# Optimization experiments

Measured on AMD Instinct MI355X. Metric: run time of the kernel, lower is better.

Reference implementation:

```python
import jax, jax.numpy as jnp
import numpy as np

B, S, D, E, K = 4, 2048, 1024, 8, 2


def setup_inputs() -> dict:
    key = jax.random.key(0)
    k1, k2, k3 = jax.random.split(key, 3)
    scale = 1.0 / np.sqrt(D)
    x = jax.random.normal(k1, (B, S, D), dtype=jnp.float32)
    Wg = jax.random.normal(k2, (D, E), dtype=jnp.float32) * scale
    bg = jnp.zeros((E,), dtype=jnp.float32)
    We = jax.random.normal(k3, (E, D, D), dtype=jnp.float32) * scale
    be = jnp.zeros((E, D), dtype=jnp.float32)
    return {"x": x, "Wg": Wg, "bg": bg, "We": We, "be": be}


def reference(x, Wg, bg, We, be):
    # gate scores: [B, S, E]
    gate_scores = jnp.einsum("bsd,de->bse", x, Wg) + bg
    topk_values, topk_indices = jax.lax.top_k(gate_scores, K)
    # mask: -inf everywhere except at top-k indices (where value == score)
    sel = jax.nn.one_hot(topk_indices, E, dtype=jnp.bool_).any(axis=-2)  # [B,S,E]
    masked = jnp.where(sel, gate_scores, -jnp.inf)
    gate_weights = jax.nn.softmax(masked, axis=-1)  # [B,S,E]
    # dense all-expert compute, as in the original: [B,S,E,D]
    expert_outputs = jnp.einsum("bsd,edh->bseh", x, We) + be
    fused = jnp.einsum("bse,bseh->bsh", gate_weights, expert_outputs)
    return fused
```

## Files before the change

kernel.cpp:

```cpp
#include <hip/hip_runtime.h>
#include <stdint.h>

#define NTOK   8192
#define DIM    1024
#define NEXP   8
#define MAXP   8192

#define BM 128
#define BN 128
#define BK 32

typedef float    f32x4  __attribute__((ext_vector_type(4)));
typedef __bf16   bf16x8 __attribute__((ext_vector_type(8)));
typedef _Float16 h16x8  __attribute__((ext_vector_type(8)));

typedef __attribute__((address_space(1))) const void* gas_ptr;
typedef __attribute__((address_space(3))) void*       las_ptr;

__device__ __forceinline__ unsigned short f32_to_bf16(float f) {
  union { float f; unsigned int u; } v; v.f = f;
  unsigned int u = v.u;
  unsigned int r = (u + 0x7FFFu + ((u >> 16) & 1u)) >> 16;
  return (unsigned short)r;
}

__global__ __launch_bounds__(256) void prep_kernel(
    const float* __restrict__ We, unsigned short* __restrict__ Wf,
    const float* __restrict__ x, const float* __restrict__ Wg,
    const float* __restrict__ bg, unsigned short* __restrict__ Xbf,
    int* __restrict__ tok_ee, float2* __restrict__ tok_w) {
  __shared__ float tile[64][65];
  const int bid = blockIdx.x;
  if (bid < 2048) {
    const int e  = bid >> 8;
    const int d0 = ((bid >> 4) & 15) * 64;
    const int h0 = (bid & 15) * 64;
    const int t  = threadIdx.x;
    const int tx = t & 63, ty = t >> 6;
    const float* src = We + (size_t)e * DIM * DIM;
#pragma unroll
    for (int i = 0; i < 16; ++i) {
      int d = ty + i * 4;
      tile[d][tx] = src[(size_t)(d0 + d) * DIM + (h0 + tx)];
    }
    __syncthreads();
    const int nt    = h0 >> 7;
    const int rbase = h0 & 64;
    const int hl    = t >> 2;
    const int k8    = t & 3;
#pragma unroll
    for (int reg = 0; reg < 2; ++reg) {
      const int kt = (d0 >> 5) + reg;
      unsigned int pk[4];
#pragma unroll
      for (int q = 0; q < 4; ++q) {
        int dl = reg * 32 + k8 * 8 + q * 2;
        pk[q] = (unsigned int)f32_to_bf16(tile[dl][hl]) |
                ((unsigned int)f32_to_bf16(tile[dl + 1][hl]) << 16);
      }
      size_t base = (((size_t)(e * 8 + nt) * 32 + kt) << 12) +
                    (size_t)(rbase + hl) * 32 + k8 * 8;
      *(uint4*)&Wf[base] = make_uint4(pk[0], pk[1], pk[2], pk[3]);
    }
    return;
  }
  const int blk  = bid - 2048;
  const int wave = threadIdx.x >> 6;
  const int lane = threadIdx.x & 63;
  const int tok0 = blk * 16 + wave * 4;

  float xs[4][16];
#pragma unroll
  for (int t = 0; t < 4; ++t) {
    const float* xr = x + (size_t)(tok0 + t) * DIM + lane * 16;
#pragma unroll
    for (int i = 0; i < 4; ++i)
      *(f32x4*)&xs[t][i * 4] = *(const f32x4*)(xr + i * 4);
  }
#pragma unroll
  for (int t = 0; t < 4; ++t) {
    unsigned int pk[8];
#pragma unroll
    for (int i = 0; i < 8; ++i)
      pk[i] = (unsigned int)f32_to_bf16(xs[t][2 * i]) |
              ((unsigned int)f32_to_bf16(xs[t][2 * i + 1]) << 16);
    uint4* xb = (uint4*)(Xbf + (size_t)(tok0 + t) * DIM + lane * 16);
    xb[0] = make_uint4(pk[0], pk[1], pk[2], pk[3]);
    xb[1] = make_uint4(pk[4], pk[5], pk[6], pk[7]);
  }

  double acc[4][8];
#pragma unroll
  for (int t = 0; t < 4; ++t)
#pragma unroll
    for (int e = 0; e < 8; ++e) acc[t][e] = 0.0;

  const float* wr = Wg + (size_t)(lane * 16) * NEXP;
#pragma unroll
  for (int i = 0; i < 16; ++i) {
    f32x4 wa = *(const f32x4*)(wr + i * 8);
    f32x4 wb = *(const f32x4*)(wr + i * 8 + 4);
    double w0 = wa[0], w1 = wa[1], w2 = wa[2], w3 = wa[3];
    double w4 = wb[0], w5 = wb[1], w6 = wb[2], w7 = wb[3];
#pragma unroll
    for (int t = 0; t < 4; ++t) {
      double xd = (double)xs[t][i];
      acc[t][0] += xd * w0; acc[t][1] += xd * w1;
      acc[t][2] += xd * w2; acc[t][3] += xd * w3;
      acc[t][4] += xd * w4; acc[t][5] += xd * w5;
      acc[t][6] += xd * w6; acc[t][7] += xd * w7;
    }
  }
#pragma unroll
  for (int m = 1; m < 64; m <<= 1)
#pragma unroll
    for (int t = 0; t < 4; ++t)
#pragma unroll
      for (int e = 0; e < 8; ++e) acc[t][e] += __shfl_xor(acc[t][e], m, 64);

  if (lane == 0) {
#pragma unroll
    for (int t = 0; t < 4; ++t) {
      float s[8];
#pragma unroll
      for (int e = 0; e < 8; ++e) s[e] = (float)acc[t][e] + bg[e];
      int i0 = 0; float v0 = s[0];
#pragma unroll
      for (int e = 1; e < 8; ++e) if (s[e] > v0) { v0 = s[e]; i0 = e; }
      int i1 = -1; float v1 = -3.4e38f;
#pragma unroll
      for (int e = 0; e < 8; ++e) if (e != i0 && s[e] > v1) { v1 = s[e]; i1 = e; }
      float t1 = expf(v1 - v0);
      float den = 1.0f + t1;
      tok_ee[tok0 + t] = i0 | (i1 << 8);
      tok_w[tok0 + t]  = make_float2(1.0f / den, t1 / den);
    }
  }
}

__global__ __launch_bounds__(1024) void compact_kernel(
    const int* __restrict__ tok_ee, const float2* __restrict__ tok_w,
    int* __restrict__ counts, int* __restrict__ pair_token,
    float* __restrict__ pair_w) {
  __shared__ int wave_cnt[16];
  __shared__ int wave_off[16];
  const int e = blockIdx.x;
  const int tid = threadIdx.x, wave = tid >> 6, lane = tid & 63;
  int base = 0;
  for (int c = 0; c < NTOK / 1024; ++c) {
    const int t = c * 1024 + tid;
    const int p = tok_ee[t];
    const bool m0 = ((p & 255) == e);
    const bool m1 = (((p >> 8) & 255) == e);
    const unsigned long long m = __ballot(m0 || m1);
    const int pre = __popcll(m & ((1ull << lane) - 1ull));
    if (lane == 0) wave_cnt[wave] = __popcll(m);
    __syncthreads();
    if (tid == 0) {
      int s = base;
      for (int w = 0; w < 16; ++w) { wave_off[w] = s; s += wave_cnt[w]; }
      base = s;
    }
    __syncthreads();
    if (m0 || m1) {
      const float2 w = tok_w[t];
      const int slot = wave_off[wave] + pre;
      pair_token[e * MAXP + slot] = (t << 1) | (m1 ? 1 : 0);
      pair_w[e * MAXP + slot]     = m1 ? w.y : w.x;
    }
    __syncthreads();
  }
  if (tid == 0) counts[e] = base;
}

__global__ __launch_bounds__(256) void moe_gemm(
    const unsigned short* __restrict__ Xbf, const unsigned short* __restrict__ Wf,
    const float* __restrict__ be, const int* __restrict__ counts,
    const int* __restrict__ pair_token, const float* __restrict__ pair_w,
    _Float16* __restrict__ part, float* __restrict__ Y, int use_part) {
  const int id  = blockIdx.x;
  const int e   = id & 7;
  const int nt  = (id >> 3) & 7;
  const int n0  = nt * BN;
  const int m0  = (id >> 6) * BM;
  const int cnt = counts[e];
  if (m0 >= cnt) return;

  __shared__ __align__(16) unsigned short As[2][BM * BK];
  __shared__ __align__(16) unsigned short Bs[2][BN * BK];

  const int tid  = threadIdx.x;
  const int wave = tid >> 6;
  const int lane = tid & 63;
  const int fm   = lane & 15;
  const int fq   = lane >> 4;
  const int wm   = wave >> 1;
  const int wn   = wave & 1;

  const int srow = wave * 32 + (lane >> 2);
  const int kc   = (lane & 3) * 8;
  const unsigned short* gA[2];
#pragma unroll
  for (int c = 0; c < 2; ++c) {
    int r  = srow + c * 16;
    int gr = m0 + r;
    int tk = (gr < cnt) ? (pair_token[e * MAXP + gr] >> 1) : 0;
    gA[c] = Xbf + (size_t)tk * DIM + kc;
  }
  const unsigned short* gB = Wf + (((size_t)(e * 8 + nt) * 32) << 12) +
                             (wave * 2) * 512 + lane * 8;

#define STAGE(buf, k0v)                                                       \
  {                                                                           \
    _Pragma("unroll") for (int c = 0; c < 2; ++c) {                           \
      __builtin_amdgcn_global_load_lds(                                       \
          (gas_ptr)(uintptr_t)(gA[c] + (k0v)),                                \
          (las_ptr)(uintptr_t)(&As[buf][(wave * 2 + c) * 512]), 16, 0, 0);    \
      __builtin_amdgcn_global_load_lds(                                       \
          (gas_ptr)(uintptr_t)(gB + (size_t)(k0v) * 128 + c * 512),           \
          (las_ptr)(uintptr_t)(&Bs[buf][(wave * 2 + c) * 512]), 16, 0, 0);    \
    }                                                                         \
  }

  f32x4 acc[4][4];
#pragma unroll
  for (int i = 0; i < 4; ++i)
#pragma unroll
    for (int j = 0; j < 4; ++j) { f32x4 z = {0.f, 0.f, 0.f, 0.f}; acc[i][j] = z; }

  STAGE(0, 0);
  int cur = 0;
  for (int k0 = 0; k0 < DIM; k0 += BK) {
    __syncthreads();
    if (k0 + BK < DIM) STAGE(cur ^ 1, k0 + BK);

    bf16x8 af[4], bfr[4];
#pragma unroll
    for (int i = 0; i < 4; ++i)
      af[i] = *(const bf16x8*)&As[cur][(wm * 64 + i * 16 + fm) * BK + fq * 8];
#pragma unroll
    for (int j = 0; j < 4; ++j)
      bfr[j] = *(const bf16x8*)&Bs[cur][(wn * 64 + j * 16 + fm) * BK + fq * 8];
#pragma unroll
    for (int i = 0; i < 4; ++i)
#pragma unroll
      for (int j = 0; j < 4; ++j)
        acc[i][j] = __builtin_amdgcn_mfma_f32_16x16x32_bf16(af[i], bfr[j],
                                                            acc[i][j], 0, 0, 0);
    cur ^= 1;
  }
#undef STAGE

  int   rowv[4][4];
  float wrow[4][4];
#pragma unroll
  for (int i = 0; i < 4; ++i)
#pragma unroll
    for (int r = 0; r < 4; ++r) {
      int gr = m0 + wm * 64 + i * 16 + fq * 4 + r;
      bool valid = gr < cnt;
      rowv[i][r] = valid ? pair_token[e * MAXP + gr] : -1;
      wrow[i][r] = valid ? pair_w[e * MAXP + gr] : 0.f;
    }
  if (use_part) {
#pragma unroll
    for (int j = 0; j < 4; ++j) {
      int col = n0 + wn * 64 + j * 16 + fm;
      float bev = be[e * DIM + col];
#pragma unroll
      for (int i = 0; i < 4; ++i)
#pragma unroll
        for (int r = 0; r < 4; ++r) {
          int v = rowv[i][r];
          if (v >= 0)
            part[(size_t)v * DIM + col] =
                (_Float16)(wrow[i][r] * (acc[i][j][r] + bev));
        }
    }
  } else {
#pragma unroll
    for (int j = 0; j < 4; ++j) {
      int col = n0 + wn * 64 + j * 16 + fm;
      float bev = be[e * DIM + col];
#pragma unroll
      for (int i = 0; i < 4; ++i)
#pragma unroll
        for (int r = 0; r < 4; ++r) {
          int v = rowv[i][r];
          if (v >= 0)
            atomicAdd(Y + (size_t)(v >> 1) * DIM + col,
                      wrow[i][r] * (acc[i][j][r] + bev));
        }
    }
  }
}

__global__ __launch_bounds__(256) void reduce_pairs(
    const _Float16* __restrict__ part, float* __restrict__ Y) {
  const int g = blockIdx.x * 256 + threadIdx.x;
  const int t = g >> 7;
  const int o = (g & 127) * 8;
  const h16x8 a = *(const h16x8*)(part + (size_t)(2 * t) * DIM + o);
  const h16x8 b = *(const h16x8*)(part + (size_t)(2 * t + 1) * DIM + o);
  float* y = Y + (size_t)t * DIM + o;
  f32x4 lo = {(float)a[0] + (float)b[0], (float)a[1] + (float)b[1],
              (float)a[2] + (float)b[2], (float)a[3] + (float)b[3]};
  f32x4 hi = {(float)a[4] + (float)b[4], (float)a[5] + (float)b[5],
              (float)a[6] + (float)b[6], (float)a[7] + (float)b[7]};
  *(f32x4*)y = lo;
  *(f32x4*)(y + 4) = hi;
}

extern "C" void kernel_launch(void* const* d_in, const int* in_sizes, int n_in,
                              void* d_out, int out_size, void* d_ws, size_t ws_size,
                              hipStream_t stream) {
  const float* x  = (const float*)d_in[0];
  const float* Wg = (const float*)d_in[1];
  const float* bg = (const float*)d_in[2];
  const float* We = (const float*)d_in[3];
  const float* be = (const float*)d_in[4];
  float* Y = (float*)d_out;

  const size_t MB = 1024 * 1024;
  char* ws = (char*)d_ws;
  unsigned short* Xbf = (unsigned short*)ws;
  unsigned short* Wf  = (unsigned short*)(ws + 16 * MB);
  const size_t part_bytes = (size_t)NTOK * 2 * DIM * 2;
  const size_t need = 32 * MB + part_bytes + 1 * MB;
  const int use_part = ws_size >= need;
  _Float16* part = (_Float16*)(ws + 32 * MB);
  char* p2 = ws + 32 * MB + (use_part ? part_bytes : 0);
  int*    counts     = (int*)p2;
  int*    pair_token = (int*)(p2 + 256);
  float*  pair_w     = (float*)(p2 + 256 + 262144);
  int*    tok_ee     = (int*)(p2 + 256 + 2 * 262144);
  float2* tok_w      = (float2*)(p2 + 256 + 2 * 262144 + 32768);

  if (!use_part)
    hipMemsetAsync(d_out, 0, (size_t)out_size * sizeof(float), stream);

  prep_kernel<<<2560, 256, 0, stream>>>(We, Wf, x, Wg, bg, Xbf, tok_ee, tok_w);
  compact_kernel<<<NEXP, 1024, 0, stream>>>(tok_ee, tok_w, counts, pair_token,
                                            pair_w);
  moe_gemm<<<8 * 8 * (NTOK / BM), 256, 0, stream>>>(
      Xbf, Wf, be, counts, pair_token, pair_w, part, Y, use_part);
  if (use_part)
    reduce_pairs<<<NTOK * DIM / 8 / 256, 256, 0, stream>>>(part, Y);
}
```

Before: 227.6 us.

## Triple-buffer LDS staging with XOR swizzle and nontemporal partial-sum traffic

Moves the MoE GEMM's global-to-LDS staging from double to triple buffering with two stages in flight. The old __syncthreads is replaced by a partial vmcnt wait plus a raw barrier, so loads overlap more compute. The k-chunk within each LDS row is XOR-swizzled on both the load side and the fragment-read side to reduce bank conflicts. Partial-sum stores and the reduce kernel's loads and stores become nontemporal to avoid cache pollution. Costs are extra LDS (lower occupancy possible) and one wasted wrap-around stage load at the tail.

```diff
diff --git a/kernel.cpp b/kernel.cpp
--- a/kernel.cpp
+++ b/kernel.cpp
@@ -186,8 +186,8 @@
   const int cnt = counts[e];
   if (m0 >= cnt) return;
 
-  __shared__ __align__(16) unsigned short As[2][BM * BK];
-  __shared__ __align__(16) unsigned short Bs[2][BN * BK];
+  __shared__ __align__(16) unsigned short As[3][BM * BK];
+  __shared__ __align__(16) unsigned short Bs[3][BN * BK];
 
   const int tid  = threadIdx.x;
   const int wave = tid >> 6;
@@ -198,7 +198,7 @@
   const int wn   = wave & 1;
 
   const int srow = wave * 32 + (lane >> 2);
-  const int kc   = (lane & 3) * 8;
+  const int kc   = (((lane & 3) ^ ((lane >> 3) & 3)) * 8);
   const unsigned short* gA[2];
 #pragma unroll
   for (int c = 0; c < 2; ++c) {
@@ -208,7 +208,7 @@
     gA[c] = Xbf + (size_t)tk * DIM + kc;
   }
   const unsigned short* gB = Wf + (((size_t)(e * 8 + nt) * 32) << 12) +
-                             (wave * 2) * 512 + lane * 8;
+                             (wave * 2) * 512 + (lane >> 2) * 32 + kc;
 
 #define STAGE(buf, k0v)                                                       \
   {                                                                           \
@@ -228,26 +228,35 @@
 #pragma unroll
     for (int j = 0; j < 4; ++j) { f32x4 z = {0.f, 0.f, 0.f, 0.f}; acc[i][j] = z; }
 
+  const int ks = ((fq ^ ((fm >> 1) & 3)) * 8);
+
   STAGE(0, 0);
+  STAGE(1, BK);
   int cur = 0;
   for (int k0 = 0; k0 < DIM; k0 += BK) {
-    __syncthreads();
-    if (k0 + BK < DIM) STAGE(cur ^ 1, k0 + BK);
+    asm volatile("s_waitcnt vmcnt(4)" ::: "memory");
+    __builtin_amdgcn_s_barrier();
+
+    int kn = k0 + 2 * BK;
+    if (kn >= DIM) kn = 0;
+    int nb = cur + 2;
+    if (nb >= 3) nb -= 3;
+    STAGE(nb, kn);
 
     bf16x8 af[4], bfr[4];
 #pragma unroll
     for (int i = 0; i < 4; ++i)
-      af[i] = *(const bf16x8*)&As[cur][(wm * 64 + i * 16 + fm) * BK + fq * 8];
+      af[i] = *(const bf16x8*)&As[cur][(wm * 64 + i * 16 + fm) * BK + ks];
 #pragma unroll
     for (int j = 0; j < 4; ++j)
-      bfr[j] = *(const bf16x8*)&Bs[cur][(wn * 64 + j * 16 + fm) * BK + fq * 8];
+      bfr[j] = *(const bf16x8*)&Bs[cur][(wn * 64 + j * 16 + fm) * BK + ks];
 #pragma unroll
     for (int i = 0; i < 4; ++i)
 #pragma unroll
       for (int j = 0; j < 4; ++j)
         acc[i][j] = __builtin_amdgcn_mfma_f32_16x16x32_bf16(af[i], bfr[j],
                                                             acc[i][j], 0, 0, 0);
-    cur ^= 1;
+    cur = (cur + 1 == 3) ? 0 : cur + 1;
   }
 #undef STAGE
 
@@ -273,8 +282,9 @@
         for (int r = 0; r < 4; ++r) {
           int v = rowv[i][r];
           if (v >= 0)
-            part[(size_t)v * DIM + col] =
-                (_Float16)(wrow[i][r] * (acc[i][j][r] + bev));
+            __builtin_nontemporal_store(
+                (_Float16)(wrow[i][r] * (acc[i][j][r] + bev)),
+                &part[(size_t)v * DIM + col]);
         }
     }
   } else {
@@ -300,15 +310,17 @@
   const int g = blockIdx.x * 256 + threadIdx.x;
   const int t = g >> 7;
   const int o = (g & 127) * 8;
-  const h16x8 a = *(const h16x8*)(part + (size_t)(2 * t) * DIM + o);
-  const h16x8 b = *(const h16x8*)(part + (size_t)(2 * t + 1) * DIM + o);
+  const h16x8 a =
+      __builtin_nontemporal_load((const h16x8*)(part + (size_t)(2 * t) * DIM + o));
+  const h16x8 b =
+      __builtin_nontemporal_load((const h16x8*)(part + (size_t)(2 * t + 1) * DIM + o));
   float* y = Y + (size_t)t * DIM + o;
   f32x4 lo = {(float)a[0] + (float)b[0], (float)a[1] + (float)b[1],
               (float)a[2] + (float)b[2], (float)a[3] + (float)b[3]};
   f32x4 hi = {(float)a[4] + (float)b[4], (float)a[5] + (float)b[5],
               (float)a[6] + (float)b[6], (float)a[7] + (float)b[7]};
-  *(f32x4*)y = lo;
-  *(f32x4*)(y + 4) = hi;
+  __builtin_nontemporal_store(lo, (f32x4*)y);
+  __builtin_nontemporal_store(hi, (f32x4*)(y + 4));
 }
 
 extern "C" void kernel_launch(void* const* d_in, const int* in_sizes, int n_in,
```

Result: faster. 221.2 us (-2.8%).
